# Kernel tuning notes

Measured on AMD Instinct MI355X. Metric: run time of the kernel, lower is better.

The kernel has to match this reference:

```python
import jax, jax.numpy as jnp
import numpy as np


def _conv2d(x, w, b, dilation=1):
    pad = dilation * (w.shape[-1] // 2)
    y = jax.lax.conv_general_dilated(x, w, (1, 1), [(pad, pad), (pad, pad)],
                                     rhs_dilation=(dilation, dilation),
                                     dimension_numbers=("NCHW", "OIHW", "NCHW"))
    return y + b[None, :, None, None]


def _bn(x, gamma, beta, mean, var):
    # eval-mode BatchNorm2d, eps=1e-5
    inv = gamma / jnp.sqrt(var + 1e-5)
    return (x - mean[None, :, None, None]) * inv[None, :, None, None] + beta[None, :, None, None]


def _frft2d(x, angles):
    # Faithful port of the source frft2d, including the quirk that
    # temp[shft, :] indexes the BATCH dim: since shft is a permutation of
    # 0..N-1, the net effect is that batch entries 0..N-1 get (i)fft'd along
    # axis -2 and entries >= N are untouched.
    temp = jnp.swapaxes(x, -1, -2)
    BC = temp.shape[0]
    for a in angles:
        a = a % 4
        N = temp.shape[-2]
        sN = np.float32(np.sqrt(N))
        mask = (jnp.arange(BC) < N)[:, None, None]
        if a == 1:
            temp = jnp.where(mask, jnp.fft.fft(temp, axis=-2) / sN, temp)
        elif a == 2:
            temp = jnp.flip(temp, axis=-2)
        elif a == 3:
            temp = jnp.where(mask, jnp.fft.ifft(temp, axis=-2) * sN, temp)
        temp = jnp.swapaxes(temp, -1, -2)
    return temp


def setup_inputs() -> dict:
    key = jax.random.key(0)
    ks = jax.random.split(key, 12)
    B, C, H, W = 4, 64, 256, 256
    f = lambda k, shape, s=0.1: jax.random.normal(k, shape, dtype=jnp.float32) * s
    z1 = jnp.zeros((1,), jnp.float32)
    o1 = jnp.ones((1,), jnp.float32)
    return {
        "x": jax.random.normal(ks[0], (B, C, H, W), dtype=jnp.float32),
        "kernel_map": jnp.ones((H, W), dtype=jnp.float32),
        "theta_w": f(ks[1], (1, 1, 3, 3)), "theta_b": z1,
        "phase_w": f(ks[2], (1, 1, 3, 3)), "phase_b": z1,
        "phase_gamma": o1, "phase_beta": z1, "phase_mean": z1, "phase_var": o1,
        "amp_w": f(ks[3], (1, 1, 1, 1)), "amp_b": z1,
        "ms_w1": f(ks[4], (1, 1, 3, 3)), "ms_b1": z1,
        "ms_w2": f(ks[5], (1, 1, 3, 3)), "ms_b2": z1,
        "ms_w3": f(ks[6], (1, 1, 3, 3)), "ms_b3": z1,
        "fc1_w": f(ks[7], (16, 1)), "fc1_b": jnp.zeros((16,), jnp.float32),
        "fc2_w": f(ks[8], (1, 16)), "fc2_b": z1,
        "fin_w": f(ks[9], (1, 6, 1, 1)), "fin_b": z1,
        "fin_gamma": o1, "fin_beta": z1, "fin_mean": z1, "fin_var": o1,
    }


def reference(x, kernel_map, theta_w, theta_b, phase_w, phase_b,
              phase_gamma, phase_beta, phase_mean, phase_var,
              amp_w, amp_b, ms_w1, ms_b1, ms_w2, ms_b2, ms_w3, ms_b3,
              fc1_w, fc1_b, fc2_w, fc2_b, fin_w, fin_b,
              fin_gamma, fin_beta, fin_mean, fin_var):
    B, C, H, W = x.shape
    BC = B * C
    xf = x.reshape(BC, H, W)
    trker = jnp.clip(jax.nn.softplus(kernel_map), 1e-3, 10.0)
    # Riesz kernels, p=(1,1) => sin(pi/2)
    Y = (jnp.arange(H, dtype=jnp.float32) + 1.0)[:, None]
    X = (jnp.arange(W, dtype=jnp.float32) + 1.0)[None, :]
    sa = np.float32(np.sin(0.5 * np.pi))
    denom = jnp.sqrt((X / sa) ** 2 + (Y / sa) ** 2) + 1e-6
    dx = ((-1j) * (X / sa) / denom).astype(jnp.complex64) * trker
    dy = ((-1j) * (Y / sa) / denom).astype(jnp.complex64) * trker
    fa = _frft2d(xf.astype(jnp.complex64), [1, 1])
    R1 = jnp.abs(_frft2d(dx * fa, [-1, -1])) + 1e-6
    R2 = jnp.abs(_frft2d(dy * fa, [-1, -1])) + 1e-6
    A = jnp.sqrt(jax.nn.relu(xf ** 2 + R1 ** 2 + R2 ** 2) + 1e-6)[:, None]
    P = jnp.arctan2(jnp.sqrt(R1 ** 2 + R2 ** 2) + 1e-6, xf + 1e-6)[:, None]
    theta = jnp.arctan2(R2, R1 + 1e-6)[:, None]
    G_theta = theta * jax.nn.sigmoid(_conv2d(theta, theta_w, theta_b))
    P_prime = jax.nn.relu(_bn(_conv2d(P, phase_w, phase_b),
                              phase_gamma, phase_beta, phase_mean, phase_var))
    A_boost = A + jax.nn.relu(_conv2d(A, amp_w, amp_b))
    ms = jnp.concatenate([_conv2d(A_boost, ms_w1, ms_b1, 1),
                          _conv2d(A_boost, ms_w2, ms_b2, 2),
                          _conv2d(A_boost, ms_w3, ms_b3, 3)], axis=1)
    # adaptive_avg_pool2d to (H, W) is the identity here
    gf = jnp.mean(A_boost, axis=(2, 3))  # (BC, 1)
    gw = jax.nn.sigmoid(jax.nn.relu(gf @ fc1_w.T + fc1_b) @ fc2_w.T + fc2_b)
    gw = gw[:, :, None, None]  # (BC,1,1,1)
    fusion = jnp.concatenate([A_boost, P_prime, G_theta, ms * gw], axis=1)  # (BC,6,H,W)
    fused = _bn(_conv2d(fusion, fin_w, fin_b), fin_gamma, fin_beta, fin_mean, fin_var)
    fused = jnp.clip(jax.nn.relu(fused), 0.0, 1.0)
    return fused.reshape(B, C, H, W)
```

## Files before the change

kernel.cpp:

```cpp
#include <hip/hip_runtime.h>
#include <hip/hip_fp16.h>
#include <math.h>

#define PI_F 3.14159265358979323846f
#define ROWB 2112ull
#define IMGB (ROWB * 256ull)

__device__ __forceinline__ unsigned rev8(unsigned v){ return __brev(v) >> 24; }

__device__ __forceinline__ float2 cmulf(float2 a, float2 b){ return make_float2(a.x*b.x - a.y*b.y, a.x*b.y + a.y*b.x); }
__device__ __forceinline__ float2 cmulc(float2 a, float2 b){ return make_float2(a.x*b.x + a.y*b.y, a.y*b.x - a.x*b.y); }
__device__ __forceinline__ float2 cadd (float2 a, float2 b){ return make_float2(a.x+b.x, a.y+b.y); }
__device__ __forceinline__ float2 csub (float2 a, float2 b){ return make_float2(a.x-b.x, a.y-b.y); }
__device__ __forceinline__ float2 eix(float a){ float s, c; __sincosf(a, &s, &c); return make_float2(c, s); }
__device__ __forceinline__ float2 sx(float2 v, int d){ return make_float2(__shfl_xor(v.x, d), __shfl_xor(v.y, d)); }

__device__ __forceinline__ unsigned packh2u(float a, float b){
  return __builtin_bit_cast(unsigned, __floats2half2_rn(a, b));
}
__device__ __forceinline__ float2 unpackh2(float p){
  return __half22float2(__builtin_bit_cast(__half2, p));
}

struct Twid { float2 w, w2, t[6]; };
__device__ __forceinline__ void mktw(Twid& T, int lane){
  T.w  = eix(-(2.0f * PI_F / 256.0f) * (float)lane);
  T.w2 = cmulf(T.w, T.w);
  #pragma unroll
  for (int st = 0; st < 6; ++st){
    const int d = 32 >> st;
    T.t[st] = eix(-(PI_F / (float)d) * (float)(lane & (d - 1)));
  }
}

__device__ __forceinline__ void fft256_fwd(float2 v[4], int lane, const Twid& T){
  const float2 t0 = cadd(v[0], v[2]);
  const float2 b0 = cmulf(csub(v[0], v[2]), T.w);
  const float2 t1 = cadd(v[1], v[3]);
  const float2 w64 = make_float2(T.w.y, -T.w.x);
  const float2 b1 = cmulf(csub(v[1], v[3]), w64);
  v[0] = cadd(t0, t1);
  v[1] = cmulf(csub(t0, t1), T.w2);
  v[2] = cadd(b0, b1);
  v[3] = cmulf(csub(b0, b1), T.w2);
  #pragma unroll
  for (int st = 0; st < 6; ++st){
    const int d = 32 >> st;
    const float2 tw = T.t[st];
    const bool hi = (lane & d) != 0;
    #pragma unroll
    for (int s = 0; s < 4; ++s){
      const float2 p  = sx(v[s], d);
      const float2 bo = cmulf(csub(p, v[s]), tw);
      const float2 lo = cadd(v[s], p);
      v[s] = hi ? bo : lo;
    }
  }
}

__device__ __forceinline__ void fft256_inv(float2 v[4], int lane, const Twid& T){
  #pragma unroll
  for (int st = 0; st < 6; ++st){
    const int d = 1 << st;
    const float2 tw = T.t[5 - st];
    const bool hi = (lane & d) != 0;
    #pragma unroll
    for (int s = 0; s < 4; ++s){
      const float2 p = sx(v[s], d);
      const float2 m = cmulc(hi ? v[s] : p, tw);
      v[s] = hi ? csub(p, m) : cadd(v[s], m);
    }
  }
  const float2 m1 = cmulc(v[1], T.w2);
  const float2 m3a = cmulc(v[3], T.w2);
  const float2 n0 = cadd(v[0], m1), n1 = csub(v[0], m1);
  const float2 n2 = cadd(v[2], m3a), n3 = csub(v[2], m3a);
  const float2 m2 = cmulc(n2, T.w);
  const float2 uci = make_float2(T.w.y, T.w.x);
  const float2 m3 = cmulf(n3, uci);
  v[0] = cadd(n0, m2); v[2] = csub(n0, m2);
  v[1] = cadd(n1, m3); v[3] = csub(n1, m3);
}

__global__ __launch_bounds__(256) void k0_prep(const float* __restrict__ km,
                                               float* __restrict__ sTabS,
                                               float* __restrict__ zrow){
  const int idx = blockIdx.x * 256 + threadIdx.x;
  const int q = idx >> 8, r = idx & 255;
  const int u = rev8(q), v = rev8(r);
  const float kv = km[u * 256 + v];
  float sp = fmaxf(kv, 0.f) + log1pf(expf(-fabsf(kv)));
  sp = fminf(fmaxf(sp, 1e-3f), 10.f);
  const float fu = (float)(u + 1), fv = (float)(v + 1);
  sTabS[idx] = sp / (sqrtf(fu * fu + fv * fv) + 1e-6f) * (1.0f / 65536.0f);
  if (blockIdx.x == 0){
    zrow[threadIdx.x] = 0.f;
    zrow[threadIdx.x + 256] = 0.f;
    if (threadIdx.x < 16) zrow[threadIdx.x + 512] = 0.f;
  }
}

__global__ __launch_bounds__(256) void k1_row(const float* __restrict__ x, char* __restrict__ arena){
  const int grp = threadIdx.x >> 6, lane = threadIdx.x & 63;
  const int rs = blockIdx.x * 4 + grp;
  Twid T; mktw(T, lane);
  const float* xr = x + (size_t)rs * 256;
  float2 v[4];
  #pragma unroll
  for (int s = 0; s < 4; ++s) v[s] = make_float2(xr[lane + 64 * s], 0.f);
  fft256_fwd(v, lane, T);
  float2* S = (float2*)(arena + (size_t)rs * ROWB);
  #pragma unroll
  for (int s = 0; s < 4; ++s) S[lane + 64 * s] = v[s];
}

__global__ __launch_bounds__(256) void k2_col(char* __restrict__ arena, const float* __restrict__ sTabS){
  __shared__ float2 lds[256 * 9];
  const int tid = threadIdx.x;
  const int b  = blockIdx.x >> 5;
  const int u0 = (blockIdx.x & 31) << 3;
  char* base = arena + (size_t)b * IMGB;

  #pragma unroll
  for (int k = 0; k < 8; ++k){
    const int idx = tid + (k << 8);
    const int r = idx >> 3, cc = idx & 7;
    lds[r * 9 + (cc ^ ((r >> 3) & 7))] = *(const float2*)(base + (size_t)r * ROWB + (size_t)(u0 + cc) * 8);
  }
  __syncthreads();

  const int wv = tid >> 6, lane = tid & 63;
  Twid T; mktw(T, lane);
  const int r6 = __brev(lane) >> 26;
  float fvv[4];
  fvv[0] = (float)(4 * r6 + 0 + 1);
  fvv[1] = (float)(4 * r6 + 2 + 1);
  fvv[2] = (float)(4 * r6 + 1 + 1);
  fvv[3] = (float)(4 * r6 + 3 + 1);
  const int swb = (lane >> 3) & 7;

  uint2 res0[4], res1[4];
  #pragma unroll
  for (int cp = 0; cp < 2; ++cp){
    const int c = wv * 2 + cp;
    const int q = u0 + c;
    const int swc = c ^ swb;
    float2 F[4];
    #pragma unroll
    for (int s = 0; s < 4; ++s) F[s] = lds[(lane + 64 * s) * 9 + swc];
    fft256_fwd(F, lane, T);
    float sc[4];
    #pragma unroll
    for (int s = 0; s < 4; ++s) sc[s] = sTabS[q * 256 + lane + 64 * s];
    const float fu = (float)(rev8((unsigned)q) + 1);
    float2 G[4];
    #pragma unroll
    for (int s = 0; s < 4; ++s){ const float a = fvv[s] * sc[s]; G[s] = make_float2(a * F[s].y, -a * F[s].x); }
    fft256_inv(G, lane, T);
    #pragma unroll
    for (int s = 0; s < 4; ++s){ (cp ? res1 : res0)[s].x = packh2u(G[s].x, G[s].y); }
    #pragma unroll
    for (int s = 0; s < 4; ++s){ const float a = fu * sc[s]; G[s] = make_float2(a * F[s].y, -a * F[s].x); }
    fft256_inv(G, lane, T);
    #pragma unroll
    for (int s = 0; s < 4; ++s){ (cp ? res1 : res0)[s].y = packh2u(G[s].x, G[s].y); }
  }
  __syncthreads();
  #pragma unroll
  for (int cp = 0; cp < 2; ++cp){
    const int c = wv * 2 + cp;
    const int swc = c ^ swb;
    #pragma unroll
    for (int s = 0; s < 4; ++s){
      const uint2 rr = cp ? res1[s] : res0[s];
      lds[(lane + 64 * s) * 9 + swc] = make_float2(__uint_as_float(rr.x), __uint_as_float(rr.y));
    }
  }
  __syncthreads();
  #pragma unroll
  for (int k = 0; k < 8; ++k){
    const int idx = tid + (k << 8);
    const int r = idx >> 3, cc = idx & 7;
    *(float2*)(base + (size_t)r * ROWB + (size_t)(u0 + cc) * 8) = lds[r * 9 + (cc ^ ((r >> 3) & 7))];
  }
}

__global__ __launch_bounds__(256) void k3_rowinv(const float* __restrict__ x, char* __restrict__ arena,
    const float* __restrict__ ampw, const float* __restrict__ ampb){
  const int grp = threadIdx.x >> 6, lane = threadIdx.x & 63;
  const int rs = blockIdx.x * 4 + grp;
  Twid T; mktw(T, lane);
  char* rowb = arena + (size_t)rs * ROWB;
  float2 g1[4], g2[4];
  #pragma unroll
  for (int s = 0; s < 4; ++s){
    const float2 pk = *(const float2*)(rowb + (size_t)(lane + 64 * s) * 8);
    g1[s] = unpackh2(pk.x); g2[s] = unpackh2(pk.y);
  }
  fft256_inv(g1, lane, T);
  fft256_inv(g2, lane, T);
  const float aw = *ampw, ab = *ampb;
  const float* xr = x + (size_t)rs * 256;
  float* Arow = (float*)(rowb + 16);
  unsigned* Prow = (unsigned*)(rowb + 1072);
  #pragma unroll
  for (int s = 0; s < 4; ++s){
    const int j = lane + 64 * s;
    const float xv = xr[j];
    const float R1 = sqrtf(g1[s].x * g1[s].x + g1[s].y * g1[s].y) + 1e-6f;
    const float R2 = sqrtf(g2[s].x * g2[s].x + g2[s].y * g2[s].y) + 1e-6f;
    const float A = sqrtf(fmaxf(xv * xv + R1 * R1 + R2 * R2, 0.f) + 1e-6f);
    const float P = atan2f(sqrtf(R1 * R1 + R2 * R2) + 1e-6f, xv + 1e-6f);
    const float Th = atan2f(R2, R1 + 1e-6f);
    const float Ab = A + fmaxf(aw * A + ab, 0.f);
    Arow[j] = Ab;
    Prow[j] = packh2u(P, Th);
  }
}

__global__ __launch_bounds__(256) void kpad(char* __restrict__ arena){
  char* row = arena + (size_t)blockIdx.x * IMGB + (size_t)threadIdx.x * ROWB;
  const float4 z = make_float4(0.f, 0.f, 0.f, 0.f);
  *(float4*)(row)         = z;
  *(float4*)(row + 1040)  = z;
  *(float4*)(row + 1056)  = z;
  *(float4*)(row + 2096)  = z;
}

__global__ __launch_bounds__(256) void k4_gw(const char* __restrict__ arena,
    const float* __restrict__ fc1w, const float* __restrict__ fc1b,
    const float* __restrict__ fc2w, const float* __restrict__ fc2b,
    float* __restrict__ gw){
  __shared__ float red[256];
  const int tid = threadIdx.x;
  const float4* row = (const float4*)(arena + (size_t)blockIdx.x * IMGB + (size_t)tid * ROWB + 16);
  float s = 0.f;
  #pragma unroll 8
  for (int k = 0; k < 64; ++k){
    const float4 v = row[k];
    s += v.x + v.y + v.z + v.w;
  }
  red[tid] = s;
  __syncthreads();
  #pragma unroll
  for (int off = 128; off; off >>= 1){
    if (tid < off) red[tid] += red[tid + off];
    __syncthreads();
  }
  if (tid == 0){
    const float gf = red[0] * (1.0f / 65536.0f);
    float acc = fc2b[0];
    #pragma unroll
    for (int k = 0; k < 16; ++k)
      acc += fc2w[k] * fmaxf(gf * fc1w[k] + fc1b[k], 0.f);
    gw[blockIdx.x] = 1.f / (1.f + expf(-acc));
  }
}

__global__ __launch_bounds__(256) void k5_fuse(
    const char* __restrict__ arena, const float* __restrict__ zrowf,
    const float* __restrict__ gwp,
    const float* __restrict__ theta_w, const float* __restrict__ theta_b,
    const float* __restrict__ phase_w, const float* __restrict__ phase_b,
    const float* __restrict__ phase_gamma, const float* __restrict__ phase_beta,
    const float* __restrict__ phase_mean, const float* __restrict__ phase_var,
    const float* __restrict__ ms_w1, const float* __restrict__ ms_b1,
    const float* __restrict__ ms_w2, const float* __restrict__ ms_b2,
    const float* __restrict__ ms_w3, const float* __restrict__ ms_b3,
    const float* __restrict__ fin_w, const float* __restrict__ fin_b,
    const float* __restrict__ fin_gamma, const float* __restrict__ fin_beta,
    const float* __restrict__ fin_mean, const float* __restrict__ fin_var,
    float* __restrict__ out){
  const int z = blockIdx.z;
  const int tx = threadIdx.x & 15, ty = threadIdx.x >> 4;
  const int j0 = (blockIdx.x << 6) + (tx << 2);
  const int i0 = (blockIdx.y << 6) + (ty << 2);
  const char* img = arena + (size_t)z * IMGB;

  float tw9[9], pw9[9], w1[9], w2[9], w3[9];
  #pragma unroll
  for (int k = 0; k < 9; ++k){
    tw9[k] = theta_w[k]; pw9[k] = phase_w[k];
    w1[k] = ms_w1[k]; w2[k] = ms_w2[k]; w3[k] = ms_w3[k];
  }
  const float b1s = ms_b1[0], b2s = ms_b2[0], b3s = ms_b3[0];
  const float tbs = theta_b[0], pbs = phase_b[0];

  float4 m1[4], m2[4], m3[4], at[4], ap[4], Ac[4], Tc[4];
  #pragma unroll
  for (int oi = 0; oi < 4; ++oi){
    m1[oi] = make_float4(b1s, b1s, b1s, b1s);
    m2[oi] = make_float4(b2s, b2s, b2s, b2s);
    m3[oi] = make_float4(b3s, b3s, b3s, b3s);
    at[oi] = make_float4(tbs, tbs, tbs, tbs);
    ap[oi] = make_float4(pbs, pbs, pbs, pbs);
  }

  #pragma unroll
  for (int lr = 0; lr < 10; ++lr){
    const int ar = i0 - 3 + lr;
    const float* rowA = ((unsigned)ar < 256u) ? (const float*)(img + (size_t)ar * ROWB) : zrowf;
    const float4 va = *(const float4*)(rowA + j0);
    const float4 vb = *(const float4*)(rowA + j0 + 4);
    const float4 vc = *(const float4*)(rowA + j0 + 8);
    const float a[12] = {va.x, va.y, va.z, va.w, vb.x, vb.y, vb.z, vb.w, vc.x, vc.y, vc.z, vc.w};
    #pragma unroll
    for (int oi = 0; oi < 4; ++oi){
      const int dd = lr - 3 - oi;
      if (dd >= -1 && dd <= 1){
        const int wr = (dd + 1) * 3;
        #pragma unroll
        for (int dx = -1; dx <= 1; ++dx){
          const float w = w1[wr + dx + 1];
          m1[oi].x += w * a[4 + 0 + dx]; m1[oi].y += w * a[4 + 1 + dx];
          m1[oi].z += w * a[4 + 2 + dx]; m1[oi].w += w * a[4 + 3 + dx];
        }
      }
      if (dd == -2 || dd == 0 || dd == 2){
        const int wr = (dd / 2 + 1) * 3;
        #pragma unroll
        for (int dx = -1; dx <= 1; ++dx){
          const float w = w2[wr + dx + 1];
          m2[oi].x += w * a[4 + 0 + 2 * dx]; m2[oi].y += w * a[4 + 1 + 2 * dx];
          m2[oi].z += w * a[4 + 2 + 2 * dx]; m2[oi].w += w * a[4 + 3 + 2 * dx];
        }
      }
      if (dd == -3 || dd == 0 || dd == 3){
        const int wr = (dd / 3 + 1) * 3;
        #pragma unroll
        for (int dx = -1; dx <= 1; ++dx){
          const float w = w3[wr + dx + 1];
          m3[oi].x += w * a[4 + 0 + 3 * dx]; m3[oi].y += w * a[4 + 1 + 3 * dx];
          m3[oi].z += w * a[4 + 2 + 3 * dx]; m3[oi].w += w * a[4 + 3 + 3 * dx];
        }
      }
      if (dd == 0) Ac[oi] = make_float4(a[4], a[5], a[6], a[7]);
    }
  }

  #pragma unroll
  for (int lr = 0; lr < 6; ++lr){
    const int ar = i0 - 1 + lr;
    const unsigned* rowP = ((unsigned)ar < 256u) ? (const unsigned*)(img + (size_t)ar * ROWB + 1056)
                                                 : (const unsigned*)zrowf;
    const uint4 ua = *(const uint4*)(rowP + j0);
    const uint4 ub = *(const uint4*)(rowP + j0 + 4);
    const uint4 uc = *(const uint4*)(rowP + j0 + 8);
    const unsigned uu[12] = {ua.x, ua.y, ua.z, ua.w, ub.x, ub.y, ub.z, ub.w, uc.x, uc.y, uc.z, uc.w};
    float p[12], t[12];
    #pragma unroll
    for (int k = 0; k < 12; ++k){
      const float2 pt = unpackh2(__builtin_bit_cast(float, uu[k]));
      p[k] = pt.x; t[k] = pt.y;
    }
    #pragma unroll
    for (int oi = 0; oi < 4; ++oi){
      const int dd = lr - 1 - oi;
      if (dd >= -1 && dd <= 1){
        const int wr = (dd + 1) * 3;
        #pragma unroll
        for (int dx = -1; dx <= 1; ++dx){
          const float wp = pw9[wr + dx + 1], wt = tw9[wr + dx + 1];
          ap[oi].x += wp * p[4 + 0 + dx]; ap[oi].y += wp * p[4 + 1 + dx];
          ap[oi].z += wp * p[4 + 2 + dx]; ap[oi].w += wp * p[4 + 3 + dx];
          at[oi].x += wt * t[4 + 0 + dx]; at[oi].y += wt * t[4 + 1 + dx];
          at[oi].z += wt * t[4 + 2 + dx]; at[oi].w += wt * t[4 + 3 + dx];
        }
      }
      if (dd == 0) Tc[oi] = make_float4(t[4], t[5], t[6], t[7]);
    }
  }

  const float gwb = gwp[z];
  const float inv_p = phase_gamma[0] * rsqrtf(phase_var[0] + 1e-5f);
  const float pmean = phase_mean[0], pbeta = phase_beta[0];
  const float f0 = fin_w[0], f1 = fin_w[1], f2 = fin_w[2];
  const float f3 = fin_w[3], f4 = fin_w[4], f5 = fin_w[5];
  const float fb = fin_b[0];
  const float inv_f = fin_gamma[0] * rsqrtf(fin_var[0] + 1e-5f);
  const float fmean = fin_mean[0], fbeta = fin_beta[0];

  #pragma unroll
  for (int oi = 0; oi < 4; ++oi){
    const float mm1[4] = {m1[oi].x, m1[oi].y, m1[oi].z, m1[oi].w};
    const float mm2[4] = {m2[oi].x, m2[oi].y, m2[oi].z, m2[oi].w};
    const float mm3[4] = {m3[oi].x, m3[oi].y, m3[oi].z, m3[oi].w};
    const float tt[4]  = {at[oi].x, at[oi].y, at[oi].z, at[oi].w};
    const float pp[4]  = {ap[oi].x, ap[oi].y, ap[oi].z, ap[oi].w};
    const float ac[4]  = {Ac[oi].x, Ac[oi].y, Ac[oi].z, Ac[oi].w};
    const float tc[4]  = {Tc[oi].x, Tc[oi].y, Tc[oi].z, Tc[oi].w};
    float o4[4];
    #pragma unroll
    for (int oj = 0; oj < 4; ++oj){
      const float Gt = tc[oj] / (1.f + expf(-tt[oj]));
      const float Pp = fmaxf((pp[oj] - pmean) * inv_p + pbeta, 0.f);
      const float pre = f0 * ac[oj] + f1 * Pp + f2 * Gt
                      + gwb * (f3 * mm1[oj] + f4 * mm2[oj] + f5 * mm3[oj]) + fb;
      float o = (pre - fmean) * inv_f + fbeta;
      o4[oj] = fminf(fmaxf(o, 0.f), 1.f);
    }
    *(float4*)(out + ((size_t)(z * 256 + i0 + oi) << 8) + j0) = make_float4(o4[0], o4[1], o4[2], o4[3]);
  }
}

extern "C" void kernel_launch(void* const* d_in, const int* in_sizes, int n_in,
                              void* d_out, int out_size, void* d_ws, size_t ws_size,
                              hipStream_t stream){
  const float* x  = (const float*)d_in[0];
  const float* km = (const float*)d_in[1];

  int N = 1;
  while (N < 64){
    const size_t need = (size_t)(256 / N) * IMGB + 2112ull + 262144ull + 1024ull;
    if (need <= ws_size) break;
    N <<= 1;
  }
  const int imgsPer = 256 / N;
  const int rowsPer = imgsPer * 256;

  char*  ws    = (char*)d_ws;
  char*  arena = ws;
  float* zrow  = (float*)(ws + (size_t)imgsPer * IMGB);
  float* sTabS = (float*)(ws + (size_t)imgsPer * IMGB + 2112ull);
  float* gwbuf = (float*)(ws + (size_t)imgsPer * IMGB + 2112ull + 262144ull);

  k0_prep<<<256, 256, 0, stream>>>(km, sTabS, zrow);

  for (int s = 0; s < N; ++s){
    const float* xs = x + (size_t)s * rowsPer * 256;
    float* outs = (float*)d_out + (size_t)s * rowsPer * 256;

    k1_row<<<rowsPer / 4, 256, 0, stream>>>(xs, arena);
    k2_col<<<imgsPer * 32, 256, 0, stream>>>(arena, sTabS);
    k3_rowinv<<<rowsPer / 4, 256, 0, stream>>>(xs, arena,
        (const float*)d_in[10], (const float*)d_in[11]);
    kpad<<<imgsPer, 256, 0, stream>>>(arena);
    k4_gw<<<imgsPer, 256, 0, stream>>>(arena,
        (const float*)d_in[18], (const float*)d_in[19],
        (const float*)d_in[20], (const float*)d_in[21], gwbuf);
    k5_fuse<<<dim3(4, 4, imgsPer), 256, 0, stream>>>(
        arena, zrow, gwbuf,
        (const float*)d_in[2],  (const float*)d_in[3],
        (const float*)d_in[4],  (const float*)d_in[5],
        (const float*)d_in[6],  (const float*)d_in[7],
        (const float*)d_in[8],  (const float*)d_in[9],
        (const float*)d_in[12], (const float*)d_in[13],
        (const float*)d_in[14], (const float*)d_in[15],
        (const float*)d_in[16], (const float*)d_in[17],
        (const float*)d_in[22], (const float*)d_in[23],
        (const float*)d_in[24], (const float*)d_in[25],
        (const float*)d_in[26], (const float*)d_in[27],
        outs);
  }
}
```

Before: 404.8 us.

## Fuse global-mean reduction into inverse row FFT and use fast atan2/sigmoid

The per-image sum of A_boost is now computed inside k3_rowinv with a wave shuffle reduction and an atomicAdd into a zeroed buffer. This lets k4_gw shrink to a single tiny block and avoids re-reading the arena. atan2f is replaced by a polynomial approximation, and sigmoid divisions use v_rcp and __expf. Launch bounds hint two blocks per CU for the FFT kernels. The changes trade some precision and make the float summation order nondeterministic because of the atomics.

```diff
diff --git a/kernel.cpp b/kernel.cpp
--- a/kernel.cpp
+++ b/kernel.cpp
@@ -14,6 +14,25 @@
 __device__ __forceinline__ float2 csub (float2 a, float2 b){ return make_float2(a.x-b.x, a.y-b.y); }
 __device__ __forceinline__ float2 eix(float a){ float s, c; __sincosf(a, &s, &c); return make_float2(c, s); }
 __device__ __forceinline__ float2 sx(float2 v, int d){ return make_float2(__shfl_xor(v.x, d), __shfl_xor(v.y, d)); }
+
+__device__ __forceinline__ float frcp(float x){ float r; asm("v_rcp_f32 %0, %1" : "=v"(r) : "v"(x)); return r; }
+
+__device__ __forceinline__ float fast_atan2pos(float y, float x){
+  const float ax = fabsf(x);
+  const float mn = fminf(ax, y), mx = fmaxf(ax, y);
+  const float t  = mn * frcp(mx);
+  const float z  = t * t;
+  float p = -0.01172120f;
+  p = fmaf(p, z,  0.05265332f);
+  p = fmaf(p, z, -0.11643287f);
+  p = fmaf(p, z,  0.19354346f);
+  p = fmaf(p, z, -0.33262347f);
+  p = fmaf(p, z,  0.99997726f);
+  p = p * t;
+  p = (y > ax) ? (1.57079632679f - p) : p;
+  p = (x < 0.f) ? (3.14159265359f - p) : p;
+  return p;
+}
 
 __device__ __forceinline__ unsigned packh2u(float a, float b){
   return __builtin_bit_cast(unsigned, __floats2half2_rn(a, b));
@@ -84,7 +103,8 @@
 
 __global__ __launch_bounds__(256) void k0_prep(const float* __restrict__ km,
                                                float* __restrict__ sTabS,
-                                               float* __restrict__ zrow){
+                                               float* __restrict__ zrow,
+                                               float* __restrict__ gfsum){
   const int idx = blockIdx.x * 256 + threadIdx.x;
   const int q = idx >> 8, r = idx & 255;
   const int u = rev8(q), v = rev8(r);
@@ -97,10 +117,11 @@
     zrow[threadIdx.x] = 0.f;
     zrow[threadIdx.x + 256] = 0.f;
     if (threadIdx.x < 16) zrow[threadIdx.x + 512] = 0.f;
-  }
-}
-
-__global__ __launch_bounds__(256) void k1_row(const float* __restrict__ x, char* __restrict__ arena){
+    gfsum[threadIdx.x] = 0.f;
+  }
+}
+
+__global__ __launch_bounds__(256, 2) void k1_row(const float* __restrict__ x, char* __restrict__ arena){
   const int grp = threadIdx.x >> 6, lane = threadIdx.x & 63;
   const int rs = blockIdx.x * 4 + grp;
   Twid T; mktw(T, lane);
@@ -185,8 +206,9 @@
   }
 }
 
-__global__ __launch_bounds__(256) void k3_rowinv(const float* __restrict__ x, char* __restrict__ arena,
-    const float* __restrict__ ampw, const float* __restrict__ ampb){
+__global__ __launch_bounds__(256, 2) void k3_rowinv(const float* __restrict__ x, char* __restrict__ arena,
+    const float* __restrict__ ampw, const float* __restrict__ ampb,
+    float* __restrict__ gfsumS){
   const int grp = threadIdx.x >> 6, lane = threadIdx.x & 63;
   const int rs = blockIdx.x * 4 + grp;
   Twid T; mktw(T, lane);
@@ -203,19 +225,25 @@
   const float* xr = x + (size_t)rs * 256;
   float* Arow = (float*)(rowb + 16);
   unsigned* Prow = (unsigned*)(rowb + 1072);
+  float sum = 0.f;
   #pragma unroll
   for (int s = 0; s < 4; ++s){
     const int j = lane + 64 * s;
     const float xv = xr[j];
-    const float R1 = sqrtf(g1[s].x * g1[s].x + g1[s].y * g1[s].y) + 1e-6f;
-    const float R2 = sqrtf(g2[s].x * g2[s].x + g2[s].y * g2[s].y) + 1e-6f;
-    const float A = sqrtf(fmaxf(xv * xv + R1 * R1 + R2 * R2, 0.f) + 1e-6f);
-    const float P = atan2f(sqrtf(R1 * R1 + R2 * R2) + 1e-6f, xv + 1e-6f);
-    const float Th = atan2f(R2, R1 + 1e-6f);
-    const float Ab = A + fmaxf(aw * A + ab, 0.f);
+    const float R1 = sqrtf(fmaf(g1[s].x, g1[s].x, g1[s].y * g1[s].y)) + 1e-6f;
+    const float R2 = sqrtf(fmaf(g2[s].x, g2[s].x, g2[s].y * g2[s].y)) + 1e-6f;
+    const float rr = fmaf(R1, R1, R2 * R2);
+    const float A = sqrtf(fmaxf(fmaf(xv, xv, rr), 0.f) + 1e-6f);
+    const float P  = fast_atan2pos(sqrtf(rr) + 1e-6f, xv + 1e-6f);
+    const float Th = fast_atan2pos(R2, R1 + 1e-6f);
+    const float Ab = A + fmaxf(fmaf(aw, A, ab), 0.f);
     Arow[j] = Ab;
     Prow[j] = packh2u(P, Th);
-  }
+    sum += Ab;
+  }
+  #pragma unroll
+  for (int off = 32; off; off >>= 1) sum += __shfl_down(sum, off);
+  if (lane == 0) atomicAdd(gfsumS + (rs >> 8), sum);
 }
 
 __global__ __launch_bounds__(256) void kpad(char* __restrict__ arena){
@@ -227,33 +255,18 @@
   *(float4*)(row + 2096)  = z;
 }
 
-__global__ __launch_bounds__(256) void k4_gw(const char* __restrict__ arena,
+__global__ __launch_bounds__(256) void k4_gw(const float* __restrict__ gfsumS,
     const float* __restrict__ fc1w, const float* __restrict__ fc1b,
     const float* __restrict__ fc2w, const float* __restrict__ fc2b,
-    float* __restrict__ gw){
-  __shared__ float red[256];
-  const int tid = threadIdx.x;
-  const float4* row = (const float4*)(arena + (size_t)blockIdx.x * IMGB + (size_t)tid * ROWB + 16);
-  float s = 0.f;
-  #pragma unroll 8
-  for (int k = 0; k < 64; ++k){
-    const float4 v = row[k];
-    s += v.x + v.y + v.z + v.w;
-  }
-  red[tid] = s;
-  __syncthreads();
-  #pragma unroll
-  for (int off = 128; off; off >>= 1){
-    if (tid < off) red[tid] += red[tid + off];
-    __syncthreads();
-  }
-  if (tid == 0){
-    const float gf = red[0] * (1.0f / 65536.0f);
+    float* __restrict__ gw, int imgs){
+  const int b = threadIdx.x;
+  if (b < imgs){
+    const float gf = gfsumS[b] * (1.0f / 65536.0f);
     float acc = fc2b[0];
     #pragma unroll
     for (int k = 0; k < 16; ++k)
       acc += fc2w[k] * fmaxf(gf * fc1w[k] + fc1b[k], 0.f);
-    gw[blockIdx.x] = 1.f / (1.f + expf(-acc));
+    gw[b] = frcp(1.f + __expf(-acc));
   }
 }
 
@@ -392,7 +405,7 @@
     float o4[4];
     #pragma unroll
     for (int oj = 0; oj < 4; ++oj){
-      const float Gt = tc[oj] / (1.f + expf(-tt[oj]));
+      const float Gt = tc[oj] * frcp(1.f + __expf(-tt[oj]));
       const float Pp = fmaxf((pp[oj] - pmean) * inv_p + pbeta, 0.f);
       const float pre = f0 * ac[oj] + f1 * Pp + f2 * Gt
                       + gwb * (f3 * mm1[oj] + f4 * mm2[oj] + f5 * mm3[oj]) + fb;
@@ -411,7 +424,7 @@
 
   int N = 1;
   while (N < 64){
-    const size_t need = (size_t)(256 / N) * IMGB + 2112ull + 262144ull + 1024ull;
+    const size_t need = (size_t)(256 / N) * IMGB + 2112ull + 262144ull + 2048ull;
     if (need <= ws_size) break;
     N <<= 1;
   }
@@ -423,21 +436,23 @@
   float* zrow  = (float*)(ws + (size_t)imgsPer * IMGB);
   float* sTabS = (float*)(ws + (size_t)imgsPer * IMGB + 2112ull);
   float* gwbuf = (float*)(ws + (size_t)imgsPer * IMGB + 2112ull + 262144ull);
-
-  k0_prep<<<256, 256, 0, stream>>>(km, sTabS, zrow);
+  float* gfsum = (float*)(ws + (size_t)imgsPer * IMGB + 2112ull + 262144ull + 1024ull);
+
+  k0_prep<<<256, 256, 0, stream>>>(km, sTabS, zrow, gfsum);
 
   for (int s = 0; s < N; ++s){
     const float* xs = x + (size_t)s * rowsPer * 256;
     float* outs = (float*)d_out + (size_t)s * rowsPer * 256;
+    float* gfs  = gfsum + (size_t)s * imgsPer;
 
     k1_row<<<rowsPer / 4, 256, 0, stream>>>(xs, arena);
     k2_col<<<imgsPer * 32, 256, 0, stream>>>(arena, sTabS);
     k3_rowinv<<<rowsPer / 4, 256, 0, stream>>>(xs, arena,
-        (const float*)d_in[10], (const float*)d_in[11]);
+        (const float*)d_in[10], (const float*)d_in[11], gfs);
     kpad<<<imgsPer, 256, 0, stream>>>(arena);
-    k4_gw<<<imgsPer, 256, 0, stream>>>(arena,
+    k4_gw<<<1, 256, 0, stream>>>(gfs,
         (const float*)d_in[18], (const float*)d_in[19],
-        (const float*)d_in[20], (const float*)d_in[21], gwbuf);
+        (const float*)d_in[20], (const float*)d_in[21], gwbuf, imgsPer);
     k5_fuse<<<dim3(4, 4, imgsPer), 256, 0, stream>>>(
         arena, zrow, gwbuf,
         (const float*)d_in[2],  (const float*)d_in[3],
```

Measured after the change: 483.4 us. +19.4%, slower.
